# Kernel optimization log

Hardware: AMD Instinct MI355X
Metric: run time of the kernel (lower is better)

The kernel has to match this reference:

```python
import jax, jax.numpy as jnp
import numpy as np

N = 50000        # nodes
E = 800000       # edges (before self-loops)
F_IN = 128       # num_features
HID = 32         # hidden_size per head
HEADS = 4
CLS = 40         # num_classes
NEG_SLOPE = 0.2  # PyG GATConv default leaky_relu slope


def setup_inputs() -> dict:
    key = jax.random.key(0)
    ks = jax.random.split(key, 10)
    s = lambda k, sh: (jax.random.normal(k, sh, jnp.float32) * 0.05)
    x = jax.random.normal(ks[0], (N, F_IN), jnp.float32)
    edge_index = jax.random.randint(ks[1], (2, E), 0, N, dtype=jnp.int64)
    W1 = s(ks[2], (F_IN, HEADS * HID))
    att_src1 = s(ks[3], (HEADS, HID))
    att_dst1 = s(ks[4], (HEADS, HID))
    b1 = jnp.zeros((HEADS * HID,), jnp.float32)
    W2 = s(ks[5], (HEADS * HID, CLS))
    att_src2 = s(ks[6], (1, CLS))
    att_dst2 = s(ks[7], (1, CLS))
    b2 = jnp.zeros((CLS,), jnp.float32)
    return {"x": x, "edge_index": edge_index, "W1": W1, "att_src1": att_src1,
            "att_dst1": att_dst1, "b1": b1, "W2": W2, "att_src2": att_src2,
            "att_dst2": att_dst2, "b2": b2}


def _add_self_loops(edge_index, num_nodes):
    ar = jnp.arange(num_nodes, dtype=edge_index.dtype)
    loops = jnp.stack([ar, ar])
    return jnp.concatenate([edge_index, loops], axis=1)


def _gat_conv(x, edge_index, W, a_src, a_dst, bias, heads, concat):
    """PyG GATConv (eval mode, additive attention, self-loops already added)."""
    n = x.shape[0]
    src, dst = edge_index[0], edge_index[1]
    h = (x @ W).reshape(n, heads, -1)                 # [N, H, C]
    a_s = jnp.einsum('nhc,hc->nh', h, a_src)          # [N, H]
    a_d = jnp.einsum('nhc,hc->nh', h, a_dst)          # [N, H]
    e = jax.nn.leaky_relu(a_s[src] + a_d[dst], NEG_SLOPE)   # [E', H]
    m = jax.ops.segment_max(e, dst, num_segments=n)   # segment softmax over dst
    ex = jnp.exp(e - m[dst])
    den = jax.ops.segment_sum(ex, dst, num_segments=n)
    alpha = ex / den[dst]                             # [E', H]
    out = jax.ops.segment_sum(h[src] * alpha[:, :, None], dst, num_segments=n)
    out = out.reshape(n, -1) if concat else out.mean(axis=1)
    return out + bias


def reference(x, edge_index, W1, att_src1, att_dst1, b1, W2, att_src2, att_dst2, b2):
    ei = _add_self_loops(edge_index, x.shape[0])
    # dropout p=0 in eval -> identity
    h = jax.nn.relu(_gat_conv(x, ei, W1, att_src1, att_dst1, b1, HEADS, True))
    out = _gat_conv(h, ei, W2, att_src2, att_dst2, b2, 1, True)  # heads=1
    return out
```

## Files before the change

### kernel.cpp

```cpp
#include <hip/hip_runtime.h>
#include <cstdint>

#define NODES 50000
#define FIN   128
#define C1    128
#define HEADS 4
#define HID   32
#define CLS   40
#define SLOPE 0.2f

#define NBUCK ((NODES + 255) >> 8)
#define EPB 2048
#define BCAP 8192

__device__ __forceinline__ float lrelu(float v) { return v > 0.f ? v : SLOPE * v; }

__device__ __forceinline__ unsigned short f2bf(float f) {
    union { float f; unsigned u; } v; v.f = f;
    unsigned u = v.u;
    return (unsigned short)((u + 0x7FFFu + ((u >> 16) & 1u)) >> 16);
}
__device__ __forceinline__ float bf2f(unsigned short b) {
    union { unsigned u; float f; } v; v.u = ((unsigned)b) << 16;
    return v.f;
}
__device__ __forceinline__ float bflo(unsigned u) {
    union { unsigned x; float f; } v; v.x = u << 16; return v.f;
}
__device__ __forceinline__ float bfhi(unsigned u) {
    union { unsigned x; float f; } v; v.x = u & 0xffff0000u; return v.f;
}

typedef __attribute__((ext_vector_type(8))) short bf16x8;
typedef __attribute__((ext_vector_type(4))) float f32x4;
typedef __attribute__((ext_vector_type(4), aligned(4))) int int4a;
typedef __attribute__((ext_vector_type(2), aligned(4))) int int2a;

__global__ __launch_bounds__(256) void k_prep(const float* __restrict__ W1,
                                              const float* __restrict__ W2,
                                              unsigned short* __restrict__ w1t,
                                              unsigned short* __restrict__ w2t,
                                              int* __restrict__ bwp) {
    __shared__ unsigned short Tb[128][136];
    const int t = threadIdx.x;
#pragma unroll
    for (int i = 0; i < 64; i++) {
        int p = i * 256 + t;
        int k = p >> 7, n = p & 127;
        Tb[n][k] = f2bf(W1[(size_t)k * C1 + n]);
    }
    __syncthreads();
#pragma unroll
    for (int i = 0; i < 8; i++) {
        int p = i * 256 + t;
        int n = p >> 4, k8 = (p & 15) * 8;
        *(uint4*)(w1t + n * 128 + k8) = *(uint4*)(&Tb[n][k8]);
    }
    for (int p = t; p < CLS * 128; p += 256) {
        int n = p >> 7, k = p & 127;
        w2t[n * 128 + k] = f2bf(W2[(size_t)k * CLS + n]);
    }
    if (t < NBUCK) bwp[t] = t * BCAP;
}

__global__ __launch_bounds__(256) void k_front(const float* __restrict__ X,
                                               const unsigned short* __restrict__ w1t,
                                               const float* __restrict__ AS,
                                               const float* __restrict__ AD,
                                               unsigned short* __restrict__ h1b,
                                               float* __restrict__ as1,
                                               float* __restrict__ ad1,
                                               const int* __restrict__ src,
                                               const int* __restrict__ dst, int E,
                                               int* __restrict__ bwp,
                                               int* __restrict__ tmp, int GB1) {
    __shared__ unsigned short Asm[64][136];
    __shared__ unsigned short Wt[128][136];
    __shared__ int cnt[NBUCK];
    __shared__ int bbs[NBUCK];
    const int t = threadIdx.x;

    if (blockIdx.x >= GB1) {
        for (int i = t; i < NBUCK; i += 256) cnt[i] = 0;
        __syncthreads();
        const int e0 = (blockIdx.x - GB1) * EPB;
        int v[8], rb[8];
#pragma unroll
        for (int k = 0; k < 8; k++) {
            int e = e0 + k * 256 + t;
            rb[k] = -1;
            if (e < E) {
                int d = dst[e], s = src[e];
                int b = d >> 8;
                int r = atomicAdd(&cnt[b], 1);
                v[k] = (s << 8) | (d & 255);
                rb[k] = (r << 8) | b;
            }
        }
        __syncthreads();
        for (int i = t; i < NBUCK; i += 256) {
            int c = cnt[i];
            bbs[i] = c ? atomicAdd(&bwp[i], c) : 0;
        }
        __syncthreads();
#pragma unroll
        for (int k = 0; k < 8; k++) {
            if (rb[k] >= 0) {
                int b = rb[k] & 255;
                int r = rb[k] >> 8;
                tmp[bbs[b] + r] = v[k];
            }
        }
        return;
    }

    const int row0 = blockIdx.x * 64;
#pragma unroll
    for (int i = 0; i < 8; i++) {
        int p = i * 256 + t;
        int n = p >> 4, k8 = (p & 15) * 8;
        *(uint4*)(&Wt[n][k8]) = *(const uint4*)(w1t + n * 128 + k8);
    }
    {
        int r = t >> 2, c0 = (t & 3) * 32;
        int gr = row0 + r;
        unsigned short tb[32];
        if (gr < NODES) {
#pragma unroll
            for (int i = 0; i < 8; i++) {
                float4 v = *(const float4*)(X + (size_t)gr * FIN + c0 + i * 4);
                tb[i * 4 + 0] = f2bf(v.x); tb[i * 4 + 1] = f2bf(v.y);
                tb[i * 4 + 2] = f2bf(v.z); tb[i * 4 + 3] = f2bf(v.w);
            }
        } else {
#pragma unroll
            for (int i = 0; i < 32; i++) tb[i] = 0;
        }
#pragma unroll
        for (int i = 0; i < 4; i++) {
            uint4 pk;
            pk.x = (unsigned)tb[i*8+0] | ((unsigned)tb[i*8+1] << 16);
            pk.y = (unsigned)tb[i*8+2] | ((unsigned)tb[i*8+3] << 16);
            pk.z = (unsigned)tb[i*8+4] | ((unsigned)tb[i*8+5] << 16);
            pk.w = (unsigned)tb[i*8+6] | ((unsigned)tb[i*8+7] << 16);
            *(uint4*)(&Asm[r][c0 + i * 8]) = pk;
        }
    }
    __syncthreads();

    const int w = t >> 6, l = t & 63;
    const int lm = l & 15, quad = l >> 4;
    f32x4 acc[8];
#pragma unroll
    for (int ct = 0; ct < 8; ct++) acc[ct] = (f32x4){0.f, 0.f, 0.f, 0.f};
#pragma unroll
    for (int kt = 0; kt < 4; kt++) {
        bf16x8 a = *(const bf16x8*)(&Asm[w * 16 + lm][kt * 32 + quad * 8]);
#pragma unroll
        for (int ct = 0; ct < 8; ct++) {
            bf16x8 b = *(const bf16x8*)(&Wt[ct * 16 + lm][kt * 32 + quad * 8]);
            acc[ct] = __builtin_amdgcn_mfma_f32_16x16x32_bf16(a, b, acc[ct], 0, 0, 0);
        }
    }
    __syncthreads();
#pragma unroll
    for (int ct = 0; ct < 8; ct++)
#pragma unroll
        for (int r = 0; r < 4; r++)
            Asm[w * 16 + quad * 4 + r][ct * 16 + lm] = f2bf(acc[ct][r]);
    __syncthreads();
    {
        int r = t >> 2, c0 = (t & 3) * 32;
        int gr = row0 + r;
        if (gr < NODES) {
#pragma unroll
            for (int i = 0; i < 4; i++)
                *(uint4*)(h1b + (size_t)gr * C1 + c0 + i * 8) =
                    *(uint4*)(&Asm[r][c0 + i * 8]);
        }
    }
    {
        int r = t >> 2, h = t & 3;
        int gr = row0 + r;
        if (gr < NODES) {
            float s = 0.f, d = 0.f;
#pragma unroll
            for (int j = 0; j < 32; j++) {
                float v = bf2f(Asm[r][h * 32 + j]);
                s = fmaf(v, AS[h * HID + j], s);
                d = fmaf(v, AD[h * HID + j], d);
            }
            as1[gr * HEADS + h] = s;
            ad1[gr * HEADS + h] = d;
        }
    }
}

__global__ __launch_bounds__(256) void k_bucketB(const int* __restrict__ bwp,
                                                 const int* __restrict__ tmp,
                                                 int* __restrict__ col,
                                                 int* __restrict__ rowptr,
                                                 int* __restrict__ degarr) {
    __shared__ int degs[256];
    __shared__ int wp[256];
    __shared__ int wsum[4];
    const int b = blockIdx.x, t = threadIdx.x;
    const int n0 = b << 8;
    const int beg = b * BCAP;
    const int end = bwp[b];
    degs[t] = 0;
    __syncthreads();
    for (int e = beg + t; e < end; e += 256)
        atomicAdd(&degs[tmp[e] & 255], 1);
    __syncthreads();
    const int d = degs[t];
    int incl = d;
    const int lane = t & 63, w = t >> 6;
#pragma unroll
    for (int s = 1; s < 64; s <<= 1) {
        int u = __shfl_up(incl, s);
        if (lane >= s) incl += u;
    }
    if (lane == 63) wsum[w] = incl;
    __syncthreads();
    if (t == 0) {
        int r = 0;
#pragma unroll
        for (int i = 0; i < 4; i++) { int x = wsum[i]; wsum[i] = r; r += x; }
    }
    __syncthreads();
    const int excl = incl - d + wsum[w] + beg;
    const int nidx = n0 + t;
    if (nidx < NODES) { rowptr[nidx] = excl; degarr[nidx] = d; }
    wp[t] = excl;
    __syncthreads();
    for (int e = beg + t; e < end; e += 256) {
        int v = tmp[e];
        int p = atomicAdd(&wp[v & 255], 1);
        col[p] = v >> 8;
    }
}

__global__ __launch_bounds__(256) void k_agg1(const unsigned short* __restrict__ h1b,
                                              const float* __restrict__ as1,
                                              const float* __restrict__ ad1,
                                              const int* __restrict__ rowptr,
                                              const int* __restrict__ degarr,
                                              const int* __restrict__ col,
                                              const float* __restrict__ b1,
                                              unsigned short* __restrict__ out1) {
    int wid = (blockIdx.x * 256 + threadIdx.x) >> 6;
    if (wid >= NODES) return;
    const int lane = threadIdx.x & 63;
    const int q  = lane >> 4;
    const int ll = lane & 15;
    const int fh = ll >> 2;
    const int n = wid;
    const float adn = ad1[n * HEADS + fh];
    const int rs = rowptr[n];
    const int re = rs + degarr[n];

    float den = 0.f;
    float ac[8];
#pragma unroll
    for (int k = 0; k < 8; k++) ac[k] = 0.f;

    int base = rs;
    for (; base + 16 <= re; base += 16) {
        int4a cc = *(const int4a*)(col + base + q * 4);
        float w0 = __expf(lrelu(as1[cc.x * HEADS + fh] + adn));
        float w1 = __expf(lrelu(as1[cc.y * HEADS + fh] + adn));
        float w2 = __expf(lrelu(as1[cc.z * HEADS + fh] + adn));
        float w3 = __expf(lrelu(as1[cc.w * HEADS + fh] + adn));
        den += (w0 + w1) + (w2 + w3);
        uint4 p0 = *(const uint4*)((const char*)h1b + (((unsigned)cc.x << 8) + (unsigned)(ll << 4)));
        uint4 p1 = *(const uint4*)((const char*)h1b + (((unsigned)cc.y << 8) + (unsigned)(ll << 4)));
        uint4 p2 = *(const uint4*)((const char*)h1b + (((unsigned)cc.z << 8) + (unsigned)(ll << 4)));
        uint4 p3 = *(const uint4*)((const char*)h1b + (((unsigned)cc.w << 8) + (unsigned)(ll << 4)));
        ac[0] = fmaf(w0, bflo(p0.x), ac[0]); ac[1] = fmaf(w0, bfhi(p0.x), ac[1]);
        ac[2] = fmaf(w0, bflo(p0.y), ac[2]); ac[3] = fmaf(w0, bfhi(p0.y), ac[3]);
        ac[4] = fmaf(w0, bflo(p0.z), ac[4]); ac[5] = fmaf(w0, bfhi(p0.z), ac[5]);
        ac[6] = fmaf(w0, bflo(p0.w), ac[6]); ac[7] = fmaf(w0, bfhi(p0.w), ac[7]);
        ac[0] = fmaf(w1, bflo(p1.x), ac[0]); ac[1] = fmaf(w1, bfhi(p1.x), ac[1]);
        ac[2] = fmaf(w1, bflo(p1.y), ac[2]); ac[3] = fmaf(w1, bfhi(p1.y), ac[3]);
        ac[4] = fmaf(w1, bflo(p1.z), ac[4]); ac[5] = fmaf(w1, bfhi(p1.z), ac[5]);
        ac[6] = fmaf(w1, bflo(p1.w), ac[6]); ac[7] = fmaf(w1, bfhi(p1.w), ac[7]);
        ac[0] = fmaf(w2, bflo(p2.x), ac[0]); ac[1] = fmaf(w2, bfhi(p2.x), ac[1]);
        ac[2] = fmaf(w2, bflo(p2.y), ac[2]); ac[3] = fmaf(w2, bfhi(p2.y), ac[3]);
        ac[4] = fmaf(w2, bflo(p2.z), ac[4]); ac[5] = fmaf(w2, bfhi(p2.z), ac[5]);
        ac[6] = fmaf(w2, bflo(p2.w), ac[6]); ac[7] = fmaf(w2, bfhi(p2.w), ac[7]);
        ac[0] = fmaf(w3, bflo(p3.x), ac[0]); ac[1] = fmaf(w3, bfhi(p3.x), ac[1]);
        ac[2] = fmaf(w3, bflo(p3.y), ac[2]); ac[3] = fmaf(w3, bfhi(p3.y), ac[3]);
        ac[4] = fmaf(w3, bflo(p3.z), ac[4]); ac[5] = fmaf(w3, bfhi(p3.z), ac[5]);
        ac[6] = fmaf(w3, bflo(p3.w), ac[6]); ac[7] = fmaf(w3, bfhi(p3.w), ac[7]);
    }
    for (; base < re; base += 4) {
        int i = base + q;
        int c = (i < re) ? col[i] : n;
        float w = __expf(lrelu(as1[c * HEADS + fh] + adn));
        if (i >= re) w = 0.f;
        den += w;
        unsigned off = ((unsigned)c << 8) + (unsigned)(ll << 4);
        uint4 pk = *(const uint4*)((const char*)h1b + off);
        ac[0] = fmaf(w, bflo(pk.x), ac[0]); ac[1] = fmaf(w, bfhi(pk.x), ac[1]);
        ac[2] = fmaf(w, bflo(pk.y), ac[2]); ac[3] = fmaf(w, bfhi(pk.y), ac[3]);
        ac[4] = fmaf(w, bflo(pk.z), ac[4]); ac[5] = fmaf(w, bfhi(pk.z), ac[5]);
        ac[6] = fmaf(w, bflo(pk.w), ac[6]); ac[7] = fmaf(w, bfhi(pk.w), ac[7]);
    }
    den += __shfl_xor(den, 16);
    den += __shfl_xor(den, 32);
#pragma unroll
    for (int k = 0; k < 8; k++) {
        ac[k] += __shfl_xor(ac[k], 16);
        ac[k] += __shfl_xor(ac[k], 32);
    }
    const float wself = __expf(lrelu(as1[n * HEADS + fh] + adn));
    den += wself;
    if (q == 0) {
        unsigned offs = ((unsigned)n << 8) + (unsigned)(ll << 4);
        uint4 sp = *(const uint4*)((const char*)h1b + offs);
        float sv[8] = {bflo(sp.x), bfhi(sp.x), bflo(sp.y), bfhi(sp.y),
                       bflo(sp.z), bfhi(sp.z), bflo(sp.w), bfhi(sp.w)};
        float4 bv0 = *(const float4*)(b1 + ll * 8);
        float4 bv1 = *(const float4*)(b1 + ll * 8 + 4);
        float bb[8] = {bv0.x, bv0.y, bv0.z, bv0.w, bv1.x, bv1.y, bv1.z, bv1.w};
        unsigned short ob[8];
#pragma unroll
        for (int k = 0; k < 8; k++)
            ob[k] = f2bf(fmaxf((ac[k] + wself * sv[k]) / den + bb[k], 0.f));
        uint4 pk;
        pk.x = (unsigned)ob[0] | ((unsigned)ob[1] << 16);
        pk.y = (unsigned)ob[2] | ((unsigned)ob[3] << 16);
        pk.z = (unsigned)ob[4] | ((unsigned)ob[5] << 16);
        pk.w = (unsigned)ob[6] | ((unsigned)ob[7] << 16);
        *(uint4*)(out1 + (size_t)n * C1 + ll * 8) = pk;
    }
}

__global__ __launch_bounds__(256) void k_gemm2(const unsigned short* __restrict__ out1b,
                                               const unsigned short* __restrict__ w2t,
                                               const float* __restrict__ AS,
                                               const float* __restrict__ AD,
                                               unsigned short* __restrict__ h2b,
                                               float* __restrict__ as2,
                                               float* __restrict__ ad2) {
    __shared__ unsigned short Asm[64][136];
    __shared__ unsigned short Wt2[48][136];
    __shared__ float Cc[64][52];
    const int t = threadIdx.x;
    const int row0 = blockIdx.x * 64;

    for (int p = t; p < 8 * 136; p += 256) Wt2[40 + p / 136][p % 136] = 0;
    for (int p = t; p < 640; p += 256) {
        int n = p >> 4, k8 = (p & 15) * 8;
        *(uint4*)(&Wt2[n][k8]) = *(const uint4*)(w2t + n * 128 + k8);
    }
    {
        int r = t >> 2, c0 = (t & 3) * 32;
        int gr = row0 + r;
        if (gr < NODES) {
#pragma unroll
            for (int i = 0; i < 4; i++)
                *(uint4*)(&Asm[r][c0 + i * 8]) =
                    *(const uint4*)(out1b + (size_t)gr * C1 + c0 + i * 8);
        } else {
            uint4 z = make_uint4(0, 0, 0, 0);
#pragma unroll
            for (int i = 0; i < 4; i++) *(uint4*)(&Asm[r][c0 + i * 8]) = z;
        }
    }
    __syncthreads();

    const int w = t >> 6, l = t & 63;
    const int lm = l & 15, quad = l >> 4;
    f32x4 acc[3];
#pragma unroll
    for (int ct = 0; ct < 3; ct++) acc[ct] = (f32x4){0.f, 0.f, 0.f, 0.f};
#pragma unroll
    for (int kt = 0; kt < 4; kt++) {
        bf16x8 a = *(const bf16x8*)(&Asm[w * 16 + lm][kt * 32 + quad * 8]);
#pragma unroll
        for (int ct = 0; ct < 3; ct++) {
            bf16x8 b = *(const bf16x8*)(&Wt2[ct * 16 + lm][kt * 32 + quad * 8]);
            acc[ct] = __builtin_amdgcn_mfma_f32_16x16x32_bf16(a, b, acc[ct], 0, 0, 0);
        }
    }
    __syncthreads();
#pragma unroll
    for (int ct = 0; ct < 3; ct++)
#pragma unroll
        for (int r = 0; r < 4; r++)
            Cc[w * 16 + quad * 4 + r][ct * 16 + lm] = acc[ct][r];
    __syncthreads();
    {
        int r = t >> 2, c0 = (t & 3) * 10;
        int gr = row0 + r;
        if (gr < NODES) {
#pragma unroll
            for (int i = 0; i < 5; i++) {
                int c = c0 + i * 2;
                unsigned pk = (unsigned)f2bf(Cc[r][c]) |
                              ((unsigned)f2bf(Cc[r][c + 1]) << 16);
                *(unsigned*)(h2b + (size_t)gr * 64 + c) = pk;
            }
            float s = 0.f, d = 0.f;
#pragma unroll
            for (int j = 0; j < 10; j++) {
                float v = Cc[r][c0 + j];
                s = fmaf(v, AS[c0 + j], s);
                d = fmaf(v, AD[c0 + j], d);
            }
            s += __shfl_xor(s, 1); s += __shfl_xor(s, 2);
            d += __shfl_xor(d, 1); d += __shfl_xor(d, 2);
            if ((t & 3) == 0) { as2[gr] = s; ad2[gr] = d; }
        }
    }
}

__global__ __launch_bounds__(256) void k_agg2(const unsigned short* __restrict__ h2b,
                                              const float* __restrict__ as2,
                                              const float* __restrict__ ad2,
                                              const int* __restrict__ rowptr,
                                              const int* __restrict__ degarr,
                                              const int* __restrict__ col,
                                              const float* __restrict__ b2,
                                              float* __restrict__ out) {
    int wid = (blockIdx.x * 256 + threadIdx.x) >> 6;
    if (wid >= NODES) return;
    const int lane = threadIdx.x & 63;
    const int q8 = lane >> 3, l8 = lane & 7;
    const int n = wid;
    const float adn = ad2[n];
    const int rs = rowptr[n];
    const int re = rs + degarr[n];

    float den = 0.f;
    float ac[8];
#pragma unroll
    for (int k = 0; k < 8; k++) ac[k] = 0.f;

    int base = rs;
    for (; base + 16 <= re; base += 16) {
        int2a cc = *(const int2a*)(col + base + q8 * 2);
        float w0 = __expf(lrelu(as2[cc.x] + adn));
        float w1 = __expf(lrelu(as2[cc.y] + adn));
        den += w0 + w1;
        if (l8 < 5) {
            unsigned o0 = ((unsigned)cc.x << 7) + (unsigned)(l8 << 4);
            unsigned o1 = ((unsigned)cc.y << 7) + (unsigned)(l8 << 4);
            uint4 p0 = *(const uint4*)((const char*)h2b + o0);
            uint4 p1 = *(const uint4*)((const char*)h2b + o1);
            ac[0] = fmaf(w0, bflo(p0.x), ac[0]); ac[1] = fmaf(w0, bfhi(p0.x), ac[1]);
            ac[2] = fmaf(w0, bflo(p0.y), ac[2]); ac[3] = fmaf(w0, bfhi(p0.y), ac[3]);
            ac[4] = fmaf(w0, bflo(p0.z), ac[4]); ac[5] = fmaf(w0, bfhi(p0.z), ac[5]);
            ac[6] = fmaf(w0, bflo(p0.w), ac[6]); ac[7] = fmaf(w0, bfhi(p0.w), ac[7]);
            ac[0] = fmaf(w1, bflo(p1.x), ac[0]); ac[1] = fmaf(w1, bfhi(p1.x), ac[1]);
            ac[2] = fmaf(w1, bflo(p1.y), ac[2]); ac[3] = fmaf(w1, bfhi(p1.y), ac[3]);
            ac[4] = fmaf(w1, bflo(p1.z), ac[4]); ac[5] = fmaf(w1, bfhi(p1.z), ac[5]);
            ac[6] = fmaf(w1, bflo(p1.w), ac[6]); ac[7] = fmaf(w1, bfhi(p1.w), ac[7]);
        }
    }
    for (; base < re; base += 8) {
        int i = base + q8;
        int c = (i < re) ? col[i] : n;
        float w = __expf(lrelu(as2[c] + adn));
        if (i >= re) w = 0.f;
        den += w;
        if (l8 < 5) {
            unsigned off = ((unsigned)c << 7) + (unsigned)(l8 << 4);
            uint4 pk = *(const uint4*)((const char*)h2b + off);
            ac[0] = fmaf(w, bflo(pk.x), ac[0]); ac[1] = fmaf(w, bfhi(pk.x), ac[1]);
            ac[2] = fmaf(w, bflo(pk.y), ac[2]); ac[3] = fmaf(w, bfhi(pk.y), ac[3]);
            ac[4] = fmaf(w, bflo(pk.z), ac[4]); ac[5] = fmaf(w, bfhi(pk.z), ac[5]);
            ac[6] = fmaf(w, bflo(pk.w), ac[6]); ac[7] = fmaf(w, bfhi(pk.w), ac[7]);
        }
    }
    den += __shfl_xor(den, 8);
    den += __shfl_xor(den, 16);
    den += __shfl_xor(den, 32);
#pragma unroll
    for (int k = 0; k < 8; k++) {
        ac[k] += __shfl_xor(ac[k], 8);
        ac[k] += __shfl_xor(ac[k], 16);
        ac[k] += __shfl_xor(ac[k], 32);
    }
    const float wself = __expf(lrelu(as2[n] + adn));
    den += wself;
    if (q8 == 0 && l8 < 5) {
        unsigned offs = ((unsigned)n << 7) + (unsigned)(l8 << 4);
        uint4 sp = *(const uint4*)((const char*)h2b + offs);
        float sv[8] = {bflo(sp.x), bfhi(sp.x), bflo(sp.y), bfhi(sp.y),
                       bflo(sp.z), bfhi(sp.z), bflo(sp.w), bfhi(sp.w)};
        float4 bv0 = *(const float4*)(b2 + l8 * 8);
        float4 bv1 = *(const float4*)(b2 + l8 * 8 + 4);
        float bb[8] = {bv0.x, bv0.y, bv0.z, bv0.w, bv1.x, bv1.y, bv1.z, bv1.w};
        float o[8];
#pragma unroll
        for (int k = 0; k < 8; k++)
            o[k] = (ac[k] + wself * sv[k]) / den + bb[k];
        *(float4*)(out + (size_t)n * CLS + l8 * 8) =
            make_float4(o[0], o[1], o[2], o[3]);
        *(float4*)(out + (size_t)n * CLS + l8 * 8 + 4) =
            make_float4(o[4], o[5], o[6], o[7]);
    }
}

extern "C" void kernel_launch(void* const* d_in, const int* in_sizes, int n_in,
                              void* d_out, int out_size, void* d_ws, size_t ws_size,
                              hipStream_t stream) {
    const float* x     = (const float*)d_in[0];
    const int*   ei    = (const int*)d_in[1];
    const float* W1    = (const float*)d_in[2];
    const float* aS1   = (const float*)d_in[3];
    const float* aD1   = (const float*)d_in[4];
    const float* b1    = (const float*)d_in[5];
    const float* W2    = (const float*)d_in[6];
    const float* aS2   = (const float*)d_in[7];
    const float* aD2   = (const float*)d_in[8];
    const float* b2    = (const float*)d_in[9];
    float* out = (float*)d_out;
    const int E = in_sizes[1] / 2;
    const int* src = ei;
    const int* dst = ei + E;

    char* ws = (char*)d_ws;
    size_t off = 0;
    auto alloc = [&](size_t bytes) -> char* {
        char* p = ws + off;
        off += (bytes + 255) & ~(size_t)255;
        return p;
    };
    unsigned short* h1b  = (unsigned short*)alloc((size_t)NODES * C1 * 2);
    unsigned short* out1 = (unsigned short*)alloc((size_t)NODES * C1 * 2);
    unsigned short* h2b  = (unsigned short*)alloc((size_t)NODES * 64 * 2);
    float* as1    = (float*)alloc((size_t)NODES * HEADS * 4);
    float* ad1    = (float*)alloc((size_t)NODES * HEADS * 4);
    float* as2    = (float*)alloc((size_t)NODES * 4);
    float* ad2    = (float*)alloc((size_t)NODES * 4);
    int* rowptr   = (int*)alloc((size_t)NODES * 4);
    int* degarr   = (int*)alloc((size_t)NODES * 4);
    int* col      = (int*)alloc((size_t)NBUCK * BCAP * 4);
    int* tmp      = (int*)alloc((size_t)NBUCK * BCAP * 4);
    unsigned short* w1t = (unsigned short*)alloc((size_t)FIN * C1 * 2);
    unsigned short* w2t = (unsigned short*)alloc((size_t)CLS * 128 * 2);
    int* bwp      = (int*)alloc((size_t)NBUCK * 4);

    const int GB1 = (NODES + 63) / 64;
    const int GBA = (E + EPB - 1) / EPB;

    k_prep<<<1, 256, 0, stream>>>(W1, W2, w1t, w2t, bwp);
    k_front<<<GB1 + GBA, 256, 0, stream>>>(x, w1t, aS1, aD1, h1b, as1, ad1,
                                           src, dst, E, bwp, tmp, GB1);
    k_bucketB<<<NBUCK, 256, 0, stream>>>(bwp, tmp, col, rowptr, degarr);
    k_agg1<<<(NODES * 64) / 256, 256, 0, stream>>>(h1b, as1, ad1, rowptr, degarr,
                                                   col, b1, out1);
    k_gemm2<<<(NODES + 63) / 64, 256, 0, stream>>>(out1, w2t, aS2, aD2, h2b, as2, ad2);
    k_agg2<<<(NODES * 64) / 256, 256, 0, stream>>>(h2b, as2, ad2, rowptr, degarr,
                                                   col, b2, out);
}
```

Baseline: 205.3 us.

## Fuse layer-2 linear transform into layer-1 aggregation and parallelize weight prep

```diff
diff --git a/kernel.cpp b/kernel.cpp
--- a/kernel.cpp
+++ b/kernel.cpp
@@ -41,26 +41,26 @@
                                               unsigned short* __restrict__ w1t,
                                               unsigned short* __restrict__ w2t,
                                               int* __restrict__ bwp) {
-    __shared__ unsigned short Tb[128][136];
-    const int t = threadIdx.x;
-#pragma unroll
-    for (int i = 0; i < 64; i++) {
-        int p = i * 256 + t;
-        int k = p >> 7, n = p & 127;
-        Tb[n][k] = f2bf(W1[(size_t)k * C1 + n]);
-    }
-    __syncthreads();
-#pragma unroll
-    for (int i = 0; i < 8; i++) {
-        int p = i * 256 + t;
-        int n = p >> 4, k8 = (p & 15) * 8;
-        *(uint4*)(w1t + n * 128 + k8) = *(uint4*)(&Tb[n][k8]);
-    }
-    for (int p = t; p < CLS * 128; p += 256) {
-        int n = p >> 7, k = p & 127;
-        w2t[n * 128 + k] = f2bf(W2[(size_t)k * CLS + n]);
-    }
-    if (t < NBUCK) bwp[t] = t * BCAP;
+    const int b = blockIdx.x, t = threadIdx.x;
+    if (b < 8) {
+        __shared__ unsigned short Tb[16][136];
+        const int n0 = b * 16;
+        const int k = t & 127, g = t >> 7;
+#pragma unroll
+        for (int i = 0; i < 8; i++)
+            Tb[g * 8 + i][k] = f2bf(W1[(size_t)k * C1 + n0 + g * 8 + i]);
+        __syncthreads();
+        {
+            int nl = t >> 4, k8 = (t & 15) * 8;
+            *(uint4*)(w1t + (n0 + nl) * 128 + k8) = *(uint4*)(&Tb[nl][k8]);
+        }
+    } else {
+        for (int p = t; p < CLS * 128; p += 256) {
+            int n = p >> 7, k = p & 127;
+            w2t[n * 128 + k] = f2bf(W2[(size_t)k * CLS + n]);
+        }
+        if (t < NBUCK) bwp[t] = t * BCAP;
+    }
 }
 
 __global__ __launch_bounds__(256) void k_front(const float* __restrict__ X,
@@ -248,7 +248,12 @@
                                               const int* __restrict__ degarr,
                                               const int* __restrict__ col,
                                               const float* __restrict__ b1,
-                                              unsigned short* __restrict__ out1) {
+                                              const unsigned short* __restrict__ w2t,
+                                              const float* __restrict__ AS2,
+                                              const float* __restrict__ AD2,
+                                              unsigned short* __restrict__ h2b,
+                                              float* __restrict__ as2o,
+                                              float* __restrict__ ad2o) {
     int wid = (blockIdx.x * 256 + threadIdx.x) >> 6;
     if (wid >= NODES) return;
     const int lane = threadIdx.x & 63;
@@ -316,104 +321,59 @@
     }
     const float wself = __expf(lrelu(as1[n * HEADS + fh] + adn));
     den += wself;
-    if (q == 0) {
-        unsigned offs = ((unsigned)n << 8) + (unsigned)(ll << 4);
-        uint4 sp = *(const uint4*)((const char*)h1b + offs);
-        float sv[8] = {bflo(sp.x), bfhi(sp.x), bflo(sp.y), bfhi(sp.y),
-                       bflo(sp.z), bfhi(sp.z), bflo(sp.w), bfhi(sp.w)};
-        float4 bv0 = *(const float4*)(b1 + ll * 8);
-        float4 bv1 = *(const float4*)(b1 + ll * 8 + 4);
-        float bb[8] = {bv0.x, bv0.y, bv0.z, bv0.w, bv1.x, bv1.y, bv1.z, bv1.w};
-        unsigned short ob[8];
-#pragma unroll
-        for (int k = 0; k < 8; k++)
-            ob[k] = f2bf(fmaxf((ac[k] + wself * sv[k]) / den + bb[k], 0.f));
-        uint4 pk;
-        pk.x = (unsigned)ob[0] | ((unsigned)ob[1] << 16);
-        pk.y = (unsigned)ob[2] | ((unsigned)ob[3] << 16);
-        pk.z = (unsigned)ob[4] | ((unsigned)ob[5] << 16);
-        pk.w = (unsigned)ob[6] | ((unsigned)ob[7] << 16);
-        *(uint4*)(out1 + (size_t)n * C1 + ll * 8) = pk;
-    }
-}
-
-__global__ __launch_bounds__(256) void k_gemm2(const unsigned short* __restrict__ out1b,
-                                               const unsigned short* __restrict__ w2t,
-                                               const float* __restrict__ AS,
-                                               const float* __restrict__ AD,
-                                               unsigned short* __restrict__ h2b,
-                                               float* __restrict__ as2,
-                                               float* __restrict__ ad2) {
-    __shared__ unsigned short Asm[64][136];
-    __shared__ unsigned short Wt2[48][136];
-    __shared__ float Cc[64][52];
-    const int t = threadIdx.x;
-    const int row0 = blockIdx.x * 64;
-
-    for (int p = t; p < 8 * 136; p += 256) Wt2[40 + p / 136][p % 136] = 0;
-    for (int p = t; p < 640; p += 256) {
-        int n = p >> 4, k8 = (p & 15) * 8;
-        *(uint4*)(&Wt2[n][k8]) = *(const uint4*)(w2t + n * 128 + k8);
-    }
-    {
-        int r = t >> 2, c0 = (t & 3) * 32;
-        int gr = row0 + r;
-        if (gr < NODES) {
-#pragma unroll
-            for (int i = 0; i < 4; i++)
-                *(uint4*)(&Asm[r][c0 + i * 8]) =
-                    *(const uint4*)(out1b + (size_t)gr * C1 + c0 + i * 8);
-        } else {
-            uint4 z = make_uint4(0, 0, 0, 0);
-#pragma unroll
-            for (int i = 0; i < 4; i++) *(uint4*)(&Asm[r][c0 + i * 8]) = z;
-        }
-    }
-    __syncthreads();
-
-    const int w = t >> 6, l = t & 63;
-    const int lm = l & 15, quad = l >> 4;
-    f32x4 acc[3];
-#pragma unroll
-    for (int ct = 0; ct < 3; ct++) acc[ct] = (f32x4){0.f, 0.f, 0.f, 0.f};
-#pragma unroll
-    for (int kt = 0; kt < 4; kt++) {
-        bf16x8 a = *(const bf16x8*)(&Asm[w * 16 + lm][kt * 32 + quad * 8]);
-#pragma unroll
-        for (int ct = 0; ct < 3; ct++) {
-            bf16x8 b = *(const bf16x8*)(&Wt2[ct * 16 + lm][kt * 32 + quad * 8]);
-            acc[ct] = __builtin_amdgcn_mfma_f32_16x16x32_bf16(a, b, acc[ct], 0, 0, 0);
-        }
-    }
-    __syncthreads();
-#pragma unroll
-    for (int ct = 0; ct < 3; ct++)
-#pragma unroll
-        for (int r = 0; r < 4; r++)
-            Cc[w * 16 + quad * 4 + r][ct * 16 + lm] = acc[ct][r];
-    __syncthreads();
-    {
-        int r = t >> 2, c0 = (t & 3) * 10;
-        int gr = row0 + r;
-        if (gr < NODES) {
-#pragma unroll
-            for (int i = 0; i < 5; i++) {
-                int c = c0 + i * 2;
-                unsigned pk = (unsigned)f2bf(Cc[r][c]) |
-                              ((unsigned)f2bf(Cc[r][c + 1]) << 16);
-                *(unsigned*)(h2b + (size_t)gr * 64 + c) = pk;
-            }
-            float s = 0.f, d = 0.f;
-#pragma unroll
-            for (int j = 0; j < 10; j++) {
-                float v = Cc[r][c0 + j];
-                s = fmaf(v, AS[c0 + j], s);
-                d = fmaf(v, AD[c0 + j], d);
-            }
-            s += __shfl_xor(s, 1); s += __shfl_xor(s, 2);
-            d += __shfl_xor(d, 1); d += __shfl_xor(d, 2);
-            if ((t & 3) == 0) { as2[gr] = s; ad2[gr] = d; }
-        }
+
+    unsigned offs = ((unsigned)n << 8) + (unsigned)(ll << 4);
+    uint4 sp = *(const uint4*)((const char*)h1b + offs);
+    float sv[8] = {bflo(sp.x), bfhi(sp.x), bflo(sp.y), bfhi(sp.y),
+                   bflo(sp.z), bfhi(sp.z), bflo(sp.w), bfhi(sp.w)};
+    float4 bv0 = *(const float4*)(b1 + ll * 8);
+    float4 bv1 = *(const float4*)(b1 + ll * 8 + 4);
+    float bb[8] = {bv0.x, bv0.y, bv0.z, bv0.w, bv1.x, bv1.y, bv1.z, bv1.w};
+    const float inv = 1.f / den;
+    float r[8];
+#pragma unroll
+    for (int k = 0; k < 8; k++)
+        r[k] = fmaxf(fmaf(wself, sv[k], ac[k]) * inv + bb[k], 0.f);
+
+    const int c0 = q * 10;
+    float p[10];
+#pragma unroll
+    for (int j = 0; j < 10; j++) {
+        uint4 wv = *(const uint4*)(w2t + (c0 + j) * 128 + ll * 8);
+        float s;
+        s =      r[0] * bflo(wv.x);
+        s = fmaf(r[1], bfhi(wv.x), s);
+        s = fmaf(r[2], bflo(wv.y), s);
+        s = fmaf(r[3], bfhi(wv.y), s);
+        s = fmaf(r[4], bflo(wv.z), s);
+        s = fmaf(r[5], bfhi(wv.z), s);
+        s = fmaf(r[6], bflo(wv.w), s);
+        s = fmaf(r[7], bfhi(wv.w), s);
+        p[j] = s;
+    }
+#pragma unroll
+    for (int j = 0; j < 10; j++) {
+        p[j] += __shfl_xor(p[j], 1);
+        p[j] += __shfl_xor(p[j], 2);
+        p[j] += __shfl_xor(p[j], 4);
+        p[j] += __shfl_xor(p[j], 8);
+    }
+    float sp2 = 0.f, dp2 = 0.f;
+#pragma unroll
+    for (int j = 0; j < 10; j++) {
+        sp2 = fmaf(p[j], AS2[c0 + j], sp2);
+        dp2 = fmaf(p[j], AD2[c0 + j], dp2);
+    }
+    sp2 += __shfl_xor(sp2, 16); sp2 += __shfl_xor(sp2, 32);
+    dp2 += __shfl_xor(dp2, 16); dp2 += __shfl_xor(dp2, 32);
+    if (lane == 0) { as2o[n] = sp2; ad2o[n] = dp2; }
+    if (ll < 5) {
+        float ea = p[0], eb = p[1];
+#pragma unroll
+        for (int j = 1; j < 5; j++)
+            if (ll == j) { ea = p[2 * j]; eb = p[2 * j + 1]; }
+        unsigned pk = (unsigned)f2bf(ea) | ((unsigned)f2bf(eb) << 16);
+        *(unsigned*)((char*)h2b + ((size_t)n << 7) + (unsigned)(c0 * 2 + ll * 4)) = pk;
     }
 }
 
@@ -531,7 +491,6 @@
         return p;
     };
     unsigned short* h1b  = (unsigned short*)alloc((size_t)NODES * C1 * 2);
-    unsigned short* out1 = (unsigned short*)alloc((size_t)NODES * C1 * 2);
     unsigned short* h2b  = (unsigned short*)alloc((size_t)NODES * 64 * 2);
     float* as1    = (float*)alloc((size_t)NODES * HEADS * 4);
     float* ad1    = (float*)alloc((size_t)NODES * HEADS * 4);
@@ -548,13 +507,13 @@
     const int GB1 = (NODES + 63) / 64;
     const int GBA = (E + EPB - 1) / EPB;
 
-    k_prep<<<1, 256, 0, stream>>>(W1, W2, w1t, w2t, bwp);
+    k_prep<<<9, 256, 0, stream>>>(W1, W2, w1t, w2t, bwp);
     k_front<<<GB1 + GBA, 256, 0, stream>>>(x, w1t, aS1, aD1, h1b, as1, ad1,
                                            src, dst, E, bwp, tmp, GB1);
     k_bucketB<<<NBUCK, 256, 0, stream>>>(bwp, tmp, col, rowptr, degarr);
     k_agg1<<<(NODES * 64) / 256, 256, 0, stream>>>(h1b, as1, ad1, rowptr, degarr,
-                                                   col, b1, out1);
-    k_gemm2<<<(NODES + 63) / 64, 256, 0, stream>>>(out1, w2t, aS2, aD2, h2b, as2, ad2);
+                                                   col, b1, w2t, aS2, aD2,
+                                                   h2b, as2, ad2);
     k_agg2<<<(NODES * 64) / 256, 256, 0, stream>>>(h2b, as2, ad2, rowptr, degarr,
                                                    col, b2, out);
 }
```

After: 207.0 us. No clear change (+0.8%).
